# Optimization experiments

Measured on AMD Instinct MI355X. Metric: run time of the kernel, lower is better.

Reference implementation:

```python
import jax, jax.numpy as jnp
import numpy as np

N_NODES = 50000


def _gcn_conv(x, W, b, src, dst, n):
    # GCNConv (PyG semantics): x' = D^-1/2 (A + I) D^-1/2 (x W) + b
    h = x @ W  # [N, out]
    loop = jnp.arange(n, dtype=src.dtype)
    s = jnp.concatenate([src, loop])  # self-loops appended
    d = jnp.concatenate([dst, loop])
    deg = jax.ops.segment_sum(jnp.ones_like(d, dtype=h.dtype), d, num_segments=n)
    dinv = jnp.where(deg > 0, jax.lax.rsqrt(deg), 0.0)
    norm = dinv[s] * dinv[d]  # [E+N]
    msgs = norm[:, None] * h[s]  # gather: [E+N, out]
    out = jax.ops.segment_sum(msgs, d, num_segments=n)  # scatter-add
    return out + b


def setup_inputs() -> dict:
    key = jax.random.key(0)
    ks = jax.random.split(key, 6)
    n, din, dh, dout, e = N_NODES, 64, 64, 16, 1600000
    x = jax.random.normal(ks[0], (n, din), dtype=jnp.float32)
    edge_index = jax.random.randint(ks[1], (2, e), 0, n, dtype=jnp.int64)
    W1 = jax.random.normal(ks[2], (din, dh), dtype=jnp.float32) / np.sqrt(din)
    b1 = jnp.zeros((dh,), dtype=jnp.float32)
    W2 = jax.random.normal(ks[3], (dh, dout), dtype=jnp.float32) / np.sqrt(dh)
    b2 = jnp.zeros((dout,), dtype=jnp.float32)
    return {"x": x, "edge_index": edge_index, "W1": W1, "b1": b1, "W2": W2, "b2": b2}


def reference(x, edge_index, W1, b1, W2, b2):
    n = x.shape[0]
    src, dst = edge_index[0], edge_index[1]
    h = _gcn_conv(x, W1, b1, src, dst, n)
    h = jax.nn.relu(h)
    h = _gcn_conv(h, W2, b2, src, dst, n)
    return jax.nn.log_softmax(h, axis=1)
```

## Files before the change

kernel.cpp:

```cpp
#include <hip/hip_runtime.h>
#include <hip/hip_bf16.h>
#include <math.h>

#define BSHIFT 6
#define BNODES 64
#define MAXB 1024
#define SORTCAP 4096

__device__ __forceinline__ bool detect_f64(const void* edges, long long nn) {
    const long long* e64 = (const long long*)edges;
    bool ok = true;
#pragma unroll
    for (int i = 0; i < 8; ++i) {
        long long v = e64[i];
        ok = ok && (v >= 0 && v < nn);
    }
    return ok;
}

__device__ __forceinline__ float bf16lo(unsigned int u) {
    return __uint_as_float(u << 16);
}
__device__ __forceinline__ float bf16hi(unsigned int u) {
    return __uint_as_float(u & 0xFFFF0000u);
}
__device__ __forceinline__ float bf16dec(unsigned short u) {
    return __uint_as_float(((unsigned int)u) << 16);
}
__device__ __forceinline__ unsigned short bf16enc(float f) {
    __hip_bfloat16 h = __float2bfloat16(f);
    return *reinterpret_cast<unsigned short*>(&h);
}

__global__ __launch_bounds__(512) void k_hist(const void* edges, long long nn,
                                              long long E, long long epb,
                                              int nbuckets, int nblk, int* partial) {
    __shared__ int cnt[MAXB];
    int t = threadIdx.x;
    int i = blockIdx.x;
    for (int b = t; b < nbuckets; b += 512) cnt[b] = 0;
    __syncthreads();
    bool f64 = detect_f64(edges, nn);
    long long e0 = (long long)i * epb;
    long long e1 = e0 + epb; if (e1 > E) e1 = E;
    for (long long e = e0 + t; e < e1; e += 512) {
        int d = f64 ? (int)((const long long*)edges)[E + e] : ((const int*)edges)[E + e];
        atomicAdd(&cnt[d >> BSHIFT], 1);
    }
    __syncthreads();
    for (int b = t; b < nbuckets; b += 512) partial[b * nblk + i] = cnt[b];
}

__global__ __launch_bounds__(256) void k_scanB(int* partial, int nblk, int* totals) {
    __shared__ int tmp[256];
    int b = blockIdx.x, t = threadIdx.x;
    int v = (t < nblk) ? partial[b * nblk + t] : 0;
    tmp[t] = v;
    __syncthreads();
    for (int off = 1; off < 256; off <<= 1) {
        int a = (t >= off) ? tmp[t - off] : 0;
        __syncthreads();
        tmp[t] += a;
        __syncthreads();
    }
    if (t < nblk) partial[b * nblk + t] = tmp[t] - v;
    if (t == 255) totals[b] = tmp[255];
}

__global__ __launch_bounds__(1024) void k_scan(const int* __restrict__ totals, int nbuckets,
                                               int* base) {
    __shared__ int tmp[MAXB];
    int t = threadIdx.x;
    int v = (t < nbuckets) ? totals[t] : 0;
    tmp[t] = v;
    __syncthreads();
    for (int off = 1; off < MAXB; off <<= 1) {
        int a = (t >= off) ? tmp[t - off] : 0;
        __syncthreads();
        tmp[t] += a;
        __syncthreads();
    }
    if (t < nbuckets) base[t] = tmp[t] - v;
}

__global__ __launch_bounds__(512) void k_place(const void* edges, long long nn,
                                               long long E, long long epb,
                                               int nbuckets, int nblk,
                                               const int* __restrict__ base,
                                               const int* __restrict__ partial,
                                               unsigned int* keys) {
    __shared__ int cur[MAXB];
    int t = threadIdx.x;
    int i = blockIdx.x;
    for (int b = t; b < nbuckets; b += 512) cur[b] = base[b] + partial[b * nblk + i];
    __syncthreads();
    bool f64 = detect_f64(edges, nn);
    long long e0 = (long long)i * epb;
    long long e1 = e0 + epb; if (e1 > E) e1 = E;
    for (long long e = e0 + t; e < e1; e += 512) {
        int s, d;
        if (f64) {
            const long long* ee = (const long long*)edges;
            s = (int)ee[e]; d = (int)ee[E + e];
        } else {
            const int* ee = (const int*)edges;
            s = ee[e]; d = ee[E + e];
        }
        int pos = atomicAdd(&cur[d >> BSHIFT], 1);
        keys[pos] = (unsigned int)s | ((unsigned int)(d & (BNODES - 1)) << 17);
    }
}

__global__ __launch_bounds__(256) void k_sortdeg(unsigned int* keys,
                                                 const int* __restrict__ base,
                                                 const int* __restrict__ totals,
                                                 int* rowstart, int* counts,
                                                 float* dinv, int n,
                                                 unsigned int* scratch) {
    __shared__ unsigned int kbuf[SORTCAP];
    __shared__ int hist[BNODES];
    __shared__ int cur[BNODES];
    int t = threadIdx.x;
    int bk = blockIdx.x;
    int st = base[bk], c = totals[bk];
    if (t < BNODES) hist[t] = 0;
    __syncthreads();
    bool fits = (c <= SORTCAP);
    if (fits) {
        for (int i = t; i < c; i += 256) {
            unsigned int k = keys[st + i];
            kbuf[i] = k;
            atomicAdd(&hist[k >> 17], 1);
        }
    } else {
        for (int i = t; i < c; i += 256) {
            unsigned int k = keys[st + i];
            scratch[st + i] = k;
            atomicAdd(&hist[k >> 17], 1);
        }
    }
    __syncthreads();
    if (t < 64) {
        int v = hist[t];
        int incl = v;
        for (int o = 1; o < 64; o <<= 1) {
            int other = __shfl_up(incl, o, 64);
            if (t >= o) incl += other;
        }
        int ex = incl - v;
        cur[t] = ex;
        int node = bk * BNODES + t;
        if (node < n) {
            rowstart[node] = st + ex;
            counts[node] = v;
            dinv[node] = rsqrtf((float)v + 1.0f);
        }
    }
    __syncthreads();
    if (fits) {
        for (int i = t; i < c; i += 256) {
            unsigned int k = kbuf[i];
            int pos = atomicAdd(&cur[k >> 17], 1);
            keys[st + pos] = k & 0x1FFFFu;
        }
    } else {
        for (int i = t; i < c; i += 256) {
            unsigned int k = scratch[st + i];
            int pos = atomicAdd(&cur[k >> 17], 1);
            keys[st + pos] = k & 0x1FFFFu;
        }
    }
}

__global__ __launch_bounds__(256) void k_gemm1(const float* __restrict__ x,
                                               const float* __restrict__ W,
                                               const float* __restrict__ dinv,
                                               unsigned short* __restrict__ h) {
    __shared__ float Ws[64][64];
    __shared__ float xs[16][64];
    int t = threadIdx.x;
    for (int i = t; i < 64 * 64; i += 256) Ws[i >> 6][i & 63] = W[i];
    long long row0 = (long long)blockIdx.x * 16;
    ((float4*)xs)[t] = ((const float4*)(x + row0 * 64))[t];
    __syncthreads();
    int r = t >> 4, c0 = (t & 15) * 4;
    float4 acc = {0.f, 0.f, 0.f, 0.f};
#pragma unroll
    for (int k = 0; k < 64; ++k) {
        float xv = xs[r][k];
        float4 wv = *((const float4*)&Ws[k][c0]);
        acc.x += xv * wv.x; acc.y += xv * wv.y;
        acc.z += xv * wv.z; acc.w += xv * wv.w;
    }
    float di = dinv[row0 + r];
    ushort4 pk;
    pk.x = bf16enc(di * acc.x);
    pk.y = bf16enc(di * acc.y);
    pk.z = bf16enc(di * acc.z);
    pk.w = bf16enc(di * acc.w);
    *((ushort4*)(h + (row0 + r) * 64 + c0)) = pk;
}

__global__ __launch_bounds__(256) void k_agg64(const int* __restrict__ rowstart,
                                               const int* __restrict__ counts,
                                               const unsigned int* __restrict__ srcs,
                                               const uint2* __restrict__ hb4,
                                               const float* __restrict__ dinv,
                                               const float* __restrict__ b,
                                               const float* __restrict__ W2,
                                               unsigned short* __restrict__ h2b, int n) {
    __shared__ float W2s[64 * 17];
    int t = threadIdx.x;
    for (int i = t; i < 64 * 16; i += 256) W2s[(i >> 4) * 17 + (i & 15)] = W2[i];
    __syncthreads();

    int d = (blockIdx.x * 256 + t) >> 6;
    if (d >= n) return;
    int lane = t & 63;
    unsigned int q = lane >> 4;
    unsigned int fl = lane & 15;
    float a0 = 0.f, a1 = 0.f, a2 = 0.f, a3 = 0.f;
    if (q == 0) {
        uint2 u = hb4[(unsigned int)d * 16u + fl];
        a0 = bf16lo(u.x); a1 = bf16hi(u.x); a2 = bf16lo(u.y); a3 = bf16hi(u.y);
    }
    int start = rowstart[d];
    int cnt = counts[d];
    int k = 0;
    for (; k + 32 <= cnt; k += 32) {
        unsigned int s0 = srcs[start + k + q];
        unsigned int s1 = srcs[start + k + 4 + q];
        unsigned int s2 = srcs[start + k + 8 + q];
        unsigned int s3 = srcs[start + k + 12 + q];
        unsigned int s4 = srcs[start + k + 16 + q];
        unsigned int s5 = srcs[start + k + 20 + q];
        unsigned int s6 = srcs[start + k + 24 + q];
        unsigned int s7 = srcs[start + k + 28 + q];
        uint2 u0 = hb4[s0 * 16u + fl];
        uint2 u1 = hb4[s1 * 16u + fl];
        uint2 u2 = hb4[s2 * 16u + fl];
        uint2 u3 = hb4[s3 * 16u + fl];
        uint2 u4 = hb4[s4 * 16u + fl];
        uint2 u5 = hb4[s5 * 16u + fl];
        uint2 u6 = hb4[s6 * 16u + fl];
        uint2 u7 = hb4[s7 * 16u + fl];
        a0 += bf16lo(u0.x); a1 += bf16hi(u0.x); a2 += bf16lo(u0.y); a3 += bf16hi(u0.y);
        a0 += bf16lo(u1.x); a1 += bf16hi(u1.x); a2 += bf16lo(u1.y); a3 += bf16hi(u1.y);
        a0 += bf16lo(u2.x); a1 += bf16hi(u2.x); a2 += bf16lo(u2.y); a3 += bf16hi(u2.y);
        a0 += bf16lo(u3.x); a1 += bf16hi(u3.x); a2 += bf16lo(u3.y); a3 += bf16hi(u3.y);
        a0 += bf16lo(u4.x); a1 += bf16hi(u4.x); a2 += bf16lo(u4.y); a3 += bf16hi(u4.y);
        a0 += bf16lo(u5.x); a1 += bf16hi(u5.x); a2 += bf16lo(u5.y); a3 += bf16hi(u5.y);
        a0 += bf16lo(u6.x); a1 += bf16hi(u6.x); a2 += bf16lo(u6.y); a3 += bf16hi(u6.y);
        a0 += bf16lo(u7.x); a1 += bf16hi(u7.x); a2 += bf16lo(u7.y); a3 += bf16hi(u7.y);
    }
    for (; k + 16 <= cnt; k += 16) {
        unsigned int s0 = srcs[start + k + q];
        unsigned int s1 = srcs[start + k + 4 + q];
        unsigned int s2 = srcs[start + k + 8 + q];
        unsigned int s3 = srcs[start + k + 12 + q];
        uint2 u0 = hb4[s0 * 16u + fl];
        uint2 u1 = hb4[s1 * 16u + fl];
        uint2 u2 = hb4[s2 * 16u + fl];
        uint2 u3 = hb4[s3 * 16u + fl];
        a0 += bf16lo(u0.x); a1 += bf16hi(u0.x); a2 += bf16lo(u0.y); a3 += bf16hi(u0.y);
        a0 += bf16lo(u1.x); a1 += bf16hi(u1.x); a2 += bf16lo(u1.y); a3 += bf16hi(u1.y);
        a0 += bf16lo(u2.x); a1 += bf16hi(u2.x); a2 += bf16lo(u2.y); a3 += bf16hi(u2.y);
        a0 += bf16lo(u3.x); a1 += bf16hi(u3.x); a2 += bf16lo(u3.y); a3 += bf16hi(u3.y);
    }
    for (; k + 8 <= cnt; k += 8) {
        unsigned int s0 = srcs[start + k + q];
        unsigned int s1 = srcs[start + k + 4 + q];
        uint2 u0 = hb4[s0 * 16u + fl];
        uint2 u1 = hb4[s1 * 16u + fl];
        a0 += bf16lo(u0.x); a1 += bf16hi(u0.x); a2 += bf16lo(u0.y); a3 += bf16hi(u0.y);
        a0 += bf16lo(u1.x); a1 += bf16hi(u1.x); a2 += bf16lo(u1.y); a3 += bf16hi(u1.y);
    }
    for (; k < cnt; k += 4) {
        int idx = k + (int)q;
        if (idx < cnt) {
            uint2 u0 = hb4[srcs[start + idx] * 16u + fl];
            a0 += bf16lo(u0.x); a1 += bf16hi(u0.x); a2 += bf16lo(u0.y); a3 += bf16hi(u0.y);
        }
    }
    a0 += __shfl_xor(a0, 16); a0 += __shfl_xor(a0, 32);
    a1 += __shfl_xor(a1, 16); a1 += __shfl_xor(a1, 32);
    a2 += __shfl_xor(a2, 16); a2 += __shfl_xor(a2, 32);
    a3 += __shfl_xor(a3, 16); a3 += __shfl_xor(a3, 32);
    float di = dinv[d];
    float4 bb = ((const float4*)b)[fl];
    float o0 = fmaxf(di * a0 + bb.x, 0.f);
    float o1 = fmaxf(di * a1 + bb.y, 0.f);
    float o2 = fmaxf(di * a2 + bb.z, 0.f);
    float o3 = fmaxf(di * a3 + bb.w, 0.f);

    int c = lane & 15;
    float acc = 0.f;
#pragma unroll
    for (int j = 0; j < 16; ++j) {
        int kk = (int)q * 16 + j;
        int srcl = (int)q * 20 + (j >> 2);
        float fv;
        if ((j & 3) == 0)      fv = __shfl(o0, srcl);
        else if ((j & 3) == 1) fv = __shfl(o1, srcl);
        else if ((j & 3) == 2) fv = __shfl(o2, srcl);
        else                   fv = __shfl(o3, srcl);
        acc += fv * W2s[kk * 17 + c];
    }
    acc += __shfl_xor(acc, 16);
    acc += __shfl_xor(acc, 32);
    if (lane < 16) h2b[(unsigned int)d * 16u + c] = bf16enc(di * acc);
}

__global__ __launch_bounds__(256) void k_agg16(const int* __restrict__ rowstart,
                                               const int* __restrict__ counts,
                                               const unsigned int* __restrict__ srcs,
                                               const unsigned short* __restrict__ hb,
                                               const float* __restrict__ dinv,
                                               const float* __restrict__ b,
                                               float* __restrict__ out, int n) {
    int g = (blockIdx.x * 256 + threadIdx.x) >> 4;
    if (g >= n) return;
    unsigned int f = threadIdx.x & 15;
    float acc = bf16dec(hb[(unsigned int)g * 16u + f]);
    int start = rowstart[g];
    int cnt = counts[g];
    int k = 0;
    for (; k + 8 <= cnt; k += 8) {
        unsigned int s0 = srcs[start + k];
        unsigned int s1 = srcs[start + k + 1];
        unsigned int s2 = srcs[start + k + 2];
        unsigned int s3 = srcs[start + k + 3];
        unsigned int s4 = srcs[start + k + 4];
        unsigned int s5 = srcs[start + k + 5];
        unsigned int s6 = srcs[start + k + 6];
        unsigned int s7 = srcs[start + k + 7];
        unsigned short u0 = hb[s0 * 16u + f];
        unsigned short u1 = hb[s1 * 16u + f];
        unsigned short u2 = hb[s2 * 16u + f];
        unsigned short u3 = hb[s3 * 16u + f];
        unsigned short u4 = hb[s4 * 16u + f];
        unsigned short u5 = hb[s5 * 16u + f];
        unsigned short u6 = hb[s6 * 16u + f];
        unsigned short u7 = hb[s7 * 16u + f];
        acc += bf16dec(u0); acc += bf16dec(u1); acc += bf16dec(u2); acc += bf16dec(u3);
        acc += bf16dec(u4); acc += bf16dec(u5); acc += bf16dec(u6); acc += bf16dec(u7);
    }
    for (; k < cnt; ++k) acc += bf16dec(hb[srcs[start + k] * 16u + f]);
    float v = dinv[g] * acc + b[f];
    float m = v;
#pragma unroll
    for (int o = 8; o >= 1; o >>= 1) m = fmaxf(m, __shfl_xor(m, o, 16));
    float ex = __expf(v - m);
#pragma unroll
    for (int o = 8; o >= 1; o >>= 1) ex += __shfl_xor(ex, o, 16);
    out[(unsigned int)g * 16u + f] = (v - m) - __logf(ex);
}

extern "C" void kernel_launch(void* const* d_in, const int* in_sizes, int n_in,
                              void* d_out, int out_size, void* d_ws, size_t ws_size,
                              hipStream_t stream) {
    const float* x  = (const float*)d_in[0];
    const void*  ei = d_in[1];
    const float* W1 = (const float*)d_in[2];
    const float* b1 = (const float*)d_in[3];
    const float* W2 = (const float*)d_in[4];
    const float* b2 = (const float*)d_in[5];

    long long dh  = in_sizes[3];
    long long din = in_sizes[2] / dh;
    long long n   = in_sizes[0] / din;
    long long E   = (long long)in_sizes[1] / 2;
    int nbuckets  = (int)((n + BNODES - 1) >> BSHIFT);

    long long epb = 8192;
    while ((E + epb - 1) / epb > 256) epb <<= 1;
    int nblk = (int)((E + epb - 1) / epb);

    char* ws = (char*)d_ws;
    auto alloc = [&](size_t bytes) { void* p = ws; ws += (bytes + 255) & ~255ULL; return p; };
    int*   totals   = (int*)alloc(nbuckets * 4);
    int*   base     = (int*)alloc(nbuckets * 4);
    int*   rowstart = (int*)alloc(n * 4);
    int*   counts   = (int*)alloc(n * 4);
    float* dinv     = (float*)alloc(n * 4);
    int*   partial  = (int*)alloc((size_t)nbuckets * nblk * 4);
    unsigned int* keys = (unsigned int*)alloc(E * 4);
    unsigned short* h1b  = (unsigned short*)alloc(n * 64 * 2);
    unsigned short* h2b  = (unsigned short*)alloc(n * 16 * 2);
    unsigned int* sort_scratch = (unsigned int*)h1b;

    float* out = (float*)d_out;

    k_hist<<<nblk, 512, 0, stream>>>(ei, n, E, epb, nbuckets, nblk, partial);
    k_scanB<<<nbuckets, 256, 0, stream>>>(partial, nblk, totals);
    k_scan<<<1, 1024, 0, stream>>>(totals, nbuckets, base);
    k_place<<<nblk, 512, 0, stream>>>(ei, n, E, epb, nbuckets, nblk, base, partial, keys);
    k_sortdeg<<<nbuckets, 256, 0, stream>>>(keys, base, totals, rowstart, counts,
                                            dinv, (int)n, sort_scratch);

    k_gemm1<<<(int)(n / 16), 256, 0, stream>>>(x, W1, dinv, h1b);
    k_agg64<<<(int)((n * 64 + 255) / 256), 256, 0, stream>>>(
        rowstart, counts, keys, (const uint2*)h1b, dinv, b1, W2, h2b, (int)n);

    k_agg16<<<(int)((n * 16 + 255) / 256), 256, 0, stream>>>(
        rowstart, counts, keys, h2b, dinv, b2, out, (int)n);
}
```

Measured before the change: 114.6 us.

## Fuse layer-1 GEMM into histogram launch and apply source dinv during aggregation

Layer-1 GEMM blocks now run in the same launch as the edge histogram, so the GEMM no longer waits for the degree computation and the x@W1 work overlaps the histogram. To allow that, the source-side dinv scaling moves out of the GEMM and into the layer-1 aggregation, which now gathers dinv[src] per edge and uses FMAs. The sort scratch gets its own buffer because h1b is now written before the sort. Costs: an extra per-edge dinv gather, the 32-wide unrolled loop is dropped, the histogram blocks use 256 threads instead of 512, and the workspace grows by E*4 bytes.

```diff
diff --git a/kernel.cpp b/kernel.cpp
--- a/kernel.cpp
+++ b/kernel.cpp
@@ -32,23 +32,51 @@
     return *reinterpret_cast<unsigned short*>(&h);
 }
 
-__global__ __launch_bounds__(512) void k_hist(const void* edges, long long nn,
-                                              long long E, long long epb,
-                                              int nbuckets, int nblk, int* partial) {
-    __shared__ int cnt[MAXB];
-    int t = threadIdx.x;
-    int i = blockIdx.x;
-    for (int b = t; b < nbuckets; b += 512) cnt[b] = 0;
-    __syncthreads();
-    bool f64 = detect_f64(edges, nn);
-    long long e0 = (long long)i * epb;
-    long long e1 = e0 + epb; if (e1 > E) e1 = E;
-    for (long long e = e0 + t; e < e1; e += 512) {
-        int d = f64 ? (int)((const long long*)edges)[E + e] : ((const int*)edges)[E + e];
-        atomicAdd(&cnt[d >> BSHIFT], 1);
-    }
-    __syncthreads();
-    for (int b = t; b < nbuckets; b += 512) partial[b * nblk + i] = cnt[b];
+__global__ __launch_bounds__(256) void k_hist_gemm1(const void* edges, long long nn,
+                                                    long long E, long long epb,
+                                                    int nbuckets, int nblk, int* partial,
+                                                    const float* __restrict__ x,
+                                                    const float* __restrict__ W1,
+                                                    unsigned short* __restrict__ h1b) {
+    __shared__ __align__(16) char smem[20480];
+    int t = threadIdx.x;
+    if (blockIdx.x < (unsigned int)nblk) {
+        int* cnt = (int*)smem;
+        int i = blockIdx.x;
+        for (int b = t; b < nbuckets; b += 256) cnt[b] = 0;
+        __syncthreads();
+        bool f64 = detect_f64(edges, nn);
+        long long e0 = (long long)i * epb;
+        long long e1 = e0 + epb; if (e1 > E) e1 = E;
+        for (long long e = e0 + t; e < e1; e += 256) {
+            int d = f64 ? (int)((const long long*)edges)[E + e] : ((const int*)edges)[E + e];
+            atomicAdd(&cnt[d >> BSHIFT], 1);
+        }
+        __syncthreads();
+        for (int b = t; b < nbuckets; b += 256) partial[b * nblk + i] = cnt[b];
+    } else {
+        float (*Ws)[64] = (float(*)[64])smem;
+        float (*xs)[64] = (float(*)[64])(smem + 64 * 64 * 4);
+        for (int i = t; i < 64 * 64; i += 256) Ws[i >> 6][i & 63] = W1[i];
+        long long row0 = (long long)(blockIdx.x - nblk) * 16;
+        ((float4*)xs)[t] = ((const float4*)(x + row0 * 64))[t];
+        __syncthreads();
+        int r = t >> 4, c0 = (t & 15) * 4;
+        float4 acc = {0.f, 0.f, 0.f, 0.f};
+#pragma unroll
+        for (int k = 0; k < 64; ++k) {
+            float xv = xs[r][k];
+            float4 wv = *((const float4*)&Ws[k][c0]);
+            acc.x += xv * wv.x; acc.y += xv * wv.y;
+            acc.z += xv * wv.z; acc.w += xv * wv.w;
+        }
+        ushort4 pk;
+        pk.x = bf16enc(acc.x);
+        pk.y = bf16enc(acc.y);
+        pk.z = bf16enc(acc.z);
+        pk.w = bf16enc(acc.w);
+        *((ushort4*)(h1b + (row0 + r) * 64 + c0)) = pk;
+    }
 }
 
 __global__ __launch_bounds__(256) void k_scanB(int* partial, int nblk, int* totals) {
@@ -172,35 +200,6 @@
     }
 }
 
-__global__ __launch_bounds__(256) void k_gemm1(const float* __restrict__ x,
-                                               const float* __restrict__ W,
-                                               const float* __restrict__ dinv,
-                                               unsigned short* __restrict__ h) {
-    __shared__ float Ws[64][64];
-    __shared__ float xs[16][64];
-    int t = threadIdx.x;
-    for (int i = t; i < 64 * 64; i += 256) Ws[i >> 6][i & 63] = W[i];
-    long long row0 = (long long)blockIdx.x * 16;
-    ((float4*)xs)[t] = ((const float4*)(x + row0 * 64))[t];
-    __syncthreads();
-    int r = t >> 4, c0 = (t & 15) * 4;
-    float4 acc = {0.f, 0.f, 0.f, 0.f};
-#pragma unroll
-    for (int k = 0; k < 64; ++k) {
-        float xv = xs[r][k];
-        float4 wv = *((const float4*)&Ws[k][c0]);
-        acc.x += xv * wv.x; acc.y += xv * wv.y;
-        acc.z += xv * wv.z; acc.w += xv * wv.w;
-    }
-    float di = dinv[row0 + r];
-    ushort4 pk;
-    pk.x = bf16enc(di * acc.x);
-    pk.y = bf16enc(di * acc.y);
-    pk.z = bf16enc(di * acc.z);
-    pk.w = bf16enc(di * acc.w);
-    *((ushort4*)(h + (row0 + r) * 64 + c0)) = pk;
-}
-
 __global__ __launch_bounds__(256) void k_agg64(const int* __restrict__ rowstart,
                                                const int* __restrict__ counts,
                                                const unsigned int* __restrict__ srcs,
@@ -219,74 +218,64 @@
     int lane = t & 63;
     unsigned int q = lane >> 4;
     unsigned int fl = lane & 15;
+    float di = dinv[d];
     float a0 = 0.f, a1 = 0.f, a2 = 0.f, a3 = 0.f;
     if (q == 0) {
         uint2 u = hb4[(unsigned int)d * 16u + fl];
-        a0 = bf16lo(u.x); a1 = bf16hi(u.x); a2 = bf16lo(u.y); a3 = bf16hi(u.y);
+        a0 = di * bf16lo(u.x); a1 = di * bf16hi(u.x);
+        a2 = di * bf16lo(u.y); a3 = di * bf16hi(u.y);
     }
     int start = rowstart[d];
     int cnt = counts[d];
     int k = 0;
-    for (; k + 32 <= cnt; k += 32) {
-        unsigned int s0 = srcs[start + k + q];
-        unsigned int s1 = srcs[start + k + 4 + q];
-        unsigned int s2 = srcs[start + k + 8 + q];
-        unsigned int s3 = srcs[start + k + 12 + q];
-        unsigned int s4 = srcs[start + k + 16 + q];
-        unsigned int s5 = srcs[start + k + 20 + q];
-        unsigned int s6 = srcs[start + k + 24 + q];
-        unsigned int s7 = srcs[start + k + 28 + q];
-        uint2 u0 = hb4[s0 * 16u + fl];
-        uint2 u1 = hb4[s1 * 16u + fl];
-        uint2 u2 = hb4[s2 * 16u + fl];
-        uint2 u3 = hb4[s3 * 16u + fl];
-        uint2 u4 = hb4[s4 * 16u + fl];
-        uint2 u5 = hb4[s5 * 16u + fl];
-        uint2 u6 = hb4[s6 * 16u + fl];
-        uint2 u7 = hb4[s7 * 16u + fl];
-        a0 += bf16lo(u0.x); a1 += bf16hi(u0.x); a2 += bf16lo(u0.y); a3 += bf16hi(u0.y);
-        a0 += bf16lo(u1.x); a1 += bf16hi(u1.x); a2 += bf16lo(u1.y); a3 += bf16hi(u1.y);
-        a0 += bf16lo(u2.x); a1 += bf16hi(u2.x); a2 += bf16lo(u2.y); a3 += bf16hi(u2.y);
-        a0 += bf16lo(u3.x); a1 += bf16hi(u3.x); a2 += bf16lo(u3.y); a3 += bf16hi(u3.y);
-        a0 += bf16lo(u4.x); a1 += bf16hi(u4.x); a2 += bf16lo(u4.y); a3 += bf16hi(u4.y);
-        a0 += bf16lo(u5.x); a1 += bf16hi(u5.x); a2 += bf16lo(u5.y); a3 += bf16hi(u5.y);
-        a0 += bf16lo(u6.x); a1 += bf16hi(u6.x); a2 += bf16lo(u6.y); a3 += bf16hi(u6.y);
-        a0 += bf16lo(u7.x); a1 += bf16hi(u7.x); a2 += bf16lo(u7.y); a3 += bf16hi(u7.y);
-    }
     for (; k + 16 <= cnt; k += 16) {
         unsigned int s0 = srcs[start + k + q];
         unsigned int s1 = srcs[start + k + 4 + q];
         unsigned int s2 = srcs[start + k + 8 + q];
         unsigned int s3 = srcs[start + k + 12 + q];
+        float dv0 = dinv[s0];
+        float dv1 = dinv[s1];
+        float dv2 = dinv[s2];
+        float dv3 = dinv[s3];
         uint2 u0 = hb4[s0 * 16u + fl];
         uint2 u1 = hb4[s1 * 16u + fl];
         uint2 u2 = hb4[s2 * 16u + fl];
         uint2 u3 = hb4[s3 * 16u + fl];
-        a0 += bf16lo(u0.x); a1 += bf16hi(u0.x); a2 += bf16lo(u0.y); a3 += bf16hi(u0.y);
-        a0 += bf16lo(u1.x); a1 += bf16hi(u1.x); a2 += bf16lo(u1.y); a3 += bf16hi(u1.y);
-        a0 += bf16lo(u2.x); a1 += bf16hi(u2.x); a2 += bf16lo(u2.y); a3 += bf16hi(u2.y);
-        a0 += bf16lo(u3.x); a1 += bf16hi(u3.x); a2 += bf16lo(u3.y); a3 += bf16hi(u3.y);
+        a0 = fmaf(dv0, bf16lo(u0.x), a0); a1 = fmaf(dv0, bf16hi(u0.x), a1);
+        a2 = fmaf(dv0, bf16lo(u0.y), a2); a3 = fmaf(dv0, bf16hi(u0.y), a3);
+        a0 = fmaf(dv1, bf16lo(u1.x), a0); a1 = fmaf(dv1, bf16hi(u1.x), a1);
+        a2 = fmaf(dv1, bf16lo(u1.y), a2); a3 = fmaf(dv1, bf16hi(u1.y), a3);
+        a0 = fmaf(dv2, bf16lo(u2.x), a0); a1 = fmaf(dv2, bf16hi(u2.x), a1);
+        a2 = fmaf(dv2, bf16lo(u2.y), a2); a3 = fmaf(dv2, bf16hi(u2.y), a3);
+        a0 = fmaf(dv3, bf16lo(u3.x), a0); a1 = fmaf(dv3, bf16hi(u3.x), a1);
+        a2 = fmaf(dv3, bf16lo(u3.y), a2); a3 = fmaf(dv3, bf16hi(u3.y), a3);
     }
     for (; k + 8 <= cnt; k += 8) {
         unsigned int s0 = srcs[start + k + q];
         unsigned int s1 = srcs[start + k + 4 + q];
+        float dv0 = dinv[s0];
+        float dv1 = dinv[s1];
         uint2 u0 = hb4[s0 * 16u + fl];
         uint2 u1 = hb4[s1 * 16u + fl];
-        a0 += bf16lo(u0.x); a1 += bf16hi(u0.x); a2 += bf16lo(u0.y); a3 += bf16hi(u0.y);
-        a0 += bf16lo(u1.x); a1 += bf16hi(u1.x); a2 += bf16lo(u1.y); a3 += bf16hi(u1.y);
+        a0 = fmaf(dv0, bf16lo(u0.x), a0); a1 = fmaf(dv0, bf16hi(u0.x), a1);
+        a2 = fmaf(dv0, bf16lo(u0.y), a2); a3 = fmaf(dv0, bf16hi(u0.y), a3);
+        a0 = fmaf(dv1, bf16lo(u1.x), a0); a1 = fmaf(dv1, bf16hi(u1.x), a1);
+        a2 = fmaf(dv1, bf16lo(u1.y), a2); a3 = fmaf(dv1, bf16hi(u1.y), a3);
     }
     for (; k < cnt; k += 4) {
         int idx = k + (int)q;
         if (idx < cnt) {
-            uint2 u0 = hb4[srcs[start + idx] * 16u + fl];
-            a0 += bf16lo(u0.x); a1 += bf16hi(u0.x); a2 += bf16lo(u0.y); a3 += bf16hi(u0.y);
+            unsigned int s0 = srcs[start + idx];
+            float dv0 = dinv[s0];
+            uint2 u0 = hb4[s0 * 16u + fl];
+            a0 = fmaf(dv0, bf16lo(u0.x), a0); a1 = fmaf(dv0, bf16hi(u0.x), a1);
+            a2 = fmaf(dv0, bf16lo(u0.y), a2); a3 = fmaf(dv0, bf16hi(u0.y), a3);
         }
     }
     a0 += __shfl_xor(a0, 16); a0 += __shfl_xor(a0, 32);
     a1 += __shfl_xor(a1, 16); a1 += __shfl_xor(a1, 32);
     a2 += __shfl_xor(a2, 16); a2 += __shfl_xor(a2, 32);
     a3 += __shfl_xor(a3, 16); a3 += __shfl_xor(a3, 32);
-    float di = dinv[d];
     float4 bb = ((const float4*)b)[fl];
     float o0 = fmaxf(di * a0 + bb.x, 0.f);
     float o1 = fmaxf(di * a1 + bb.y, 0.f);
@@ -375,6 +364,7 @@
     long long epb = 8192;
     while ((E + epb - 1) / epb > 256) epb <<= 1;
     int nblk = (int)((E + epb - 1) / epb);
+    int ngemm = (int)(n / 16);
 
     char* ws = (char*)d_ws;
     auto alloc = [&](size_t bytes) { void* p = ws; ws += (bytes + 255) & ~255ULL; return p; };
@@ -387,18 +377,18 @@
     unsigned int* keys = (unsigned int*)alloc(E * 4);
     unsigned short* h1b  = (unsigned short*)alloc(n * 64 * 2);
     unsigned short* h2b  = (unsigned short*)alloc(n * 16 * 2);
-    unsigned int* sort_scratch = (unsigned int*)h1b;
+    unsigned int* sort_scratch = (unsigned int*)alloc(E * 4);
 
     float* out = (float*)d_out;
 
-    k_hist<<<nblk, 512, 0, stream>>>(ei, n, E, epb, nbuckets, nblk, partial);
+    k_hist_gemm1<<<nblk + ngemm, 256, 0, stream>>>(ei, n, E, epb, nbuckets, nblk,
+                                                   partial, x, W1, h1b);
     k_scanB<<<nbuckets, 256, 0, stream>>>(partial, nblk, totals);
     k_scan<<<1, 1024, 0, stream>>>(totals, nbuckets, base);
     k_place<<<nblk, 512, 0, stream>>>(ei, n, E, epb, nbuckets, nblk, base, partial, keys);
     k_sortdeg<<<nbuckets, 256, 0, stream>>>(keys, base, totals, rowstart, counts,
                                             dinv, (int)n, sort_scratch);
 
-    k_gemm1<<<(int)(n / 16), 256, 0, stream>>>(x, W1, dinv, h1b);
     k_agg64<<<(int)((n * 64 + 255) / 256), 256, 0, stream>>>(
         rowstart, counts, keys, (const uint2*)h1b, dinv, b1, W2, h2b, (int)n);
 
```

Measured after the change: 110.6 us (median of 3 runs). 1.04x faster.
